# Kernel optimization log

Measured on AMD Instinct MI355X. Metric: run time of the kernel, lower is better.

Reference implementation:

```python
import jax, jax.numpy as jnp
import numpy as np

N = 50000
E = 800000
IN_FEATS = 128
OUT_FEATS = 64
ALPHA = 0.2  # LeakyReLU negative slope


def setup_inputs() -> dict:
    key = jax.random.key(0)
    k1, k2, k3, k4, k5 = jax.random.split(key, 5)
    h = jax.random.normal(k1, (N, IN_FEATS), dtype=jnp.float32)
    src = jax.random.randint(k2, (E,), 0, N)
    dst = jax.random.randint(k3, (E,), 0, N)
    edge_index = jnp.stack([src, dst], axis=0).astype(jnp.int64)
    # xavier_uniform with gain=1.414
    limW = 1.414 * np.sqrt(6.0 / (IN_FEATS + OUT_FEATS))
    W = jax.random.uniform(k4, (IN_FEATS, OUT_FEATS), dtype=jnp.float32, minval=-limW, maxval=limW)
    lima = 1.414 * np.sqrt(6.0 / (2 * OUT_FEATS + 1))
    a = jax.random.uniform(k5, (2 * OUT_FEATS, 1), dtype=jnp.float32, minval=-lima, maxval=lima)
    return {"h": h, "edge_index": edge_index, "W": W, "a": a}


def reference(h, edge_index, W, a):
    src, dst = edge_index[0], edge_index[1]
    Wh = h @ W                               # (N, out)
    # split attention vector: cat([Wh_src, Wh_dst]) @ a == Wh_src@a1 + Wh_dst@a2
    a1 = a[:OUT_FEATS, 0]                    # (out,)
    a2 = a[OUT_FEATS:, 0]                    # (out,)
    s1 = Wh @ a1                             # (N,)
    s2 = Wh @ a2                             # (N,)
    e = jax.nn.leaky_relu(s1[src] + s2[dst], negative_slope=ALPHA)  # (E,)
    exp_e = jnp.exp(e)
    denom = jax.ops.segment_sum(exp_e, dst, num_segments=N)          # (N,)
    attention = exp_e / denom[dst]                                   # (E,)
    # dropout p=0.0 / eval mode -> identity
    msgs = attention[:, None] * Wh[src]                              # (E, out)
    h_prime = jax.ops.segment_sum(msgs, dst, num_segments=N)         # (N, out)
    return jax.nn.elu(h_prime)
```

## Files before the change

### kernel.cpp

```cpp
#include <hip/hip_runtime.h>
#include <math.h>

#define GN 50000
#define GE 800000
#define INF 128
#define OUTF 64
#define LRELU_ALPHA 0.2f

#define BUCK_SH 6
#define BUCKW   64
#define NB      ((GN + BUCKW - 1) / BUCKW)
#define CHUNK   4096
#define NCH     ((GE + CHUNK - 1) / CHUNK)
#define CAP     1536

__device__ __forceinline__ unsigned short f32_to_bf16(float f) {
    unsigned int u = __float_as_uint(f);
    return (unsigned short)((u + 0x7fffu + ((u >> 16) & 1u)) >> 16);
}
__device__ __forceinline__ float bf16lo(unsigned int u) { return __uint_as_float(u << 16); }
__device__ __forceinline__ float bf16hi(unsigned int u) { return __uint_as_float(u & 0xffff0000u); }

__global__ __launch_bounds__(256) void k_front(const float* __restrict__ h,
                                               const float* __restrict__ W,
                                               const float* __restrict__ a,
                                               const int* __restrict__ src,
                                               const int* __restrict__ dst,
                                               unsigned short* __restrict__ Whb,
                                               float* __restrict__ s1,
                                               float* __restrict__ s2,
                                               int* __restrict__ ccount,
                                               int* __restrict__ epacked) {
    __shared__ __align__(16) float Wlds[INF * OUTF];
    int t = threadIdx.x;

    if (blockIdx.x < NB) {
        for (int i = t * 4; i < INF * OUTF; i += 256 * 4)
            *(float4*)&Wlds[i] = *(const float4*)&W[i];
        __syncthreads();

        int fg = t & 15;
        int ng = t >> 4;
        int jg = fg * 4;
        int n0 = blockIdx.x * 64 + ng * 4;

        int m0 = n0 + 0 < GN ? n0 + 0 : GN - 1;
        int m1 = n0 + 1 < GN ? n0 + 1 : GN - 1;
        int m2 = n0 + 2 < GN ? n0 + 2 : GN - 1;
        int m3 = n0 + 3 < GN ? n0 + 3 : GN - 1;
        const float* h0 = &h[m0 * INF];
        const float* h1 = &h[m1 * INF];
        const float* h2 = &h[m2 * INF];
        const float* h3 = &h[m3 * INF];

        float4 acc0 = {0.f,0.f,0.f,0.f}, acc1 = acc0, acc2 = acc0, acc3 = acc0;
        for (int kc = 0; kc < INF; kc += 4) {
            float4 hv0 = *(const float4*)&h0[kc];
            float4 hv1 = *(const float4*)&h1[kc];
            float4 hv2 = *(const float4*)&h2[kc];
            float4 hv3 = *(const float4*)&h3[kc];
            #pragma unroll
            for (int kk = 0; kk < 4; ++kk) {
                float4 wv = *(float4*)&Wlds[(kc + kk) * OUTF + jg];
                float a0 = ((const float*)&hv0)[kk];
                float a1v = ((const float*)&hv1)[kk];
                float a2v = ((const float*)&hv2)[kk];
                float a3 = ((const float*)&hv3)[kk];
                acc0.x += a0 * wv.x; acc0.y += a0 * wv.y; acc0.z += a0 * wv.z; acc0.w += a0 * wv.w;
                acc1.x += a1v * wv.x; acc1.y += a1v * wv.y; acc1.z += a1v * wv.z; acc1.w += a1v * wv.w;
                acc2.x += a2v * wv.x; acc2.y += a2v * wv.y; acc2.z += a2v * wv.z; acc2.w += a2v * wv.w;
                acc3.x += a3 * wv.x; acc3.y += a3 * wv.y; acc3.z += a3 * wv.z; acc3.w += a3 * wv.w;
            }
        }

        float4 accs[4] = {acc0, acc1, acc2, acc3};
        #pragma unroll
        for (int i = 0; i < 4; ++i) {
            if (n0 + i < GN) {
                ushort4 p;
                p.x = f32_to_bf16(accs[i].x); p.y = f32_to_bf16(accs[i].y);
                p.z = f32_to_bf16(accs[i].z); p.w = f32_to_bf16(accs[i].w);
                *(ushort4*)&Whb[(n0 + i) * OUTF + jg] = p;
            }
        }

        float4 va1 = *(const float4*)&a[jg];
        float4 va2 = *(const float4*)&a[OUTF + jg];
        float p1[4], p2[4];
        #pragma unroll
        for (int i = 0; i < 4; ++i) {
            p1[i] = accs[i].x * va1.x + accs[i].y * va1.y + accs[i].z * va1.z + accs[i].w * va1.w;
            p2[i] = accs[i].x * va2.x + accs[i].y * va2.y + accs[i].z * va2.z + accs[i].w * va2.w;
        }
        #pragma unroll
        for (int off = 8; off >= 1; off >>= 1) {
            #pragma unroll
            for (int i = 0; i < 4; ++i) {
                p1[i] += __shfl_down(p1[i], off, 16);
                p2[i] += __shfl_down(p2[i], off, 16);
            }
        }
        if (fg == 0) {
            #pragma unroll
            for (int i = 0; i < 4; ++i) {
                if (n0 + i < GN) { s1[n0 + i] = p1[i]; s2[n0 + i] = p2[i]; }
            }
        }
    } else {
        int* hist = (int*)Wlds;
        int* run  = hist + NB;
        for (int i = t; i < NB; i += 256) hist[i] = 0;
        __syncthreads();

        int base = (blockIdx.x - NB) * CHUNK;
        int pk[CHUNK / 256];
        int bb[CHUNK / 256];
        #pragma unroll
        for (int i = 0; i < CHUNK / 256; ++i) {
            int e = base + i * 256 + t;
            if (e < GE) {
                int d = dst[e];
                int b = d >> BUCK_SH;
                pk[i] = (src[e] << BUCK_SH) | (d & (BUCKW - 1));
                bb[i] = b;
                atomicAdd(&hist[b], 1);
            } else {
                bb[i] = -1;
            }
        }
        __syncthreads();
        for (int i = t; i < NB; i += 256) {
            int c = hist[i];
            if (c > 0) run[i] = i * CAP + atomicAdd(&ccount[i], c);
        }
        __syncthreads();
        #pragma unroll
        for (int i = 0; i < CHUNK / 256; ++i) {
            if (bb[i] >= 0) {
                int pos = atomicAdd(&run[bb[i]], 1);
                epacked[pos] = pk[i];
            }
        }
    }
}

__global__ __launch_bounds__(256) void k_fgather(const int* __restrict__ ccount,
                                                 const int* __restrict__ epacked,
                                                 const float* __restrict__ s1,
                                                 const float* __restrict__ s2,
                                                 const unsigned short* __restrict__ Whb,
                                                 float* __restrict__ out) {
    __shared__ int elds[CAP];
    __shared__ int sorted[CAP];
    __shared__ float exs[CAP];
    __shared__ int hist[BUCKW];
    __shared__ int cur[BUCKW];
    __shared__ int cstart[BUCKW + 1];
    __shared__ float s2l[BUCKW];

    int t = threadIdx.x;
    int b = blockIdx.x;
    int dstbase = b * BUCKW;
    int nd = GN - dstbase; if (nd > BUCKW) nd = BUCKW;

    int start = b * CAP;
    int cnt   = ccount[b];
    if (cnt > CAP) cnt = CAP;

    if (t < BUCKW) {
        hist[t] = 0;
        s2l[t] = (t < nd) ? s2[dstbase + t] : 0.f;
    }
    __syncthreads();

    float exr[CAP / 256];
    #pragma unroll
    for (int it = 0; it < CAP / 256; ++it) {
        int i = t + it * 256;
        if (i < cnt) {
            int pk = epacked[start + i];
            elds[i] = pk;
            atomicAdd(&hist[pk & (BUCKW - 1)], 1);
            float x = s1[pk >> BUCK_SH] + s2l[pk & (BUCKW - 1)];
            x = (x > 0.f) ? x : LRELU_ALPHA * x;
            exr[it] = __expf(x);
        }
    }
    __syncthreads();
    if (t < 64) {
        int v = hist[t];
        int incl = v;
        #pragma unroll
        for (int off = 1; off < 64; off <<= 1) {
            int u = __shfl_up(incl, off, 64);
            if (t >= off) incl += u;
        }
        cstart[t + 1] = incl;
        cur[t] = incl - v;
        if (t == 0) cstart[0] = 0;
    }
    __syncthreads();
    #pragma unroll
    for (int it = 0; it < CAP / 256; ++it) {
        int i = t + it * 256;
        if (i < cnt) {
            int pk = elds[i];
            int pos = atomicAdd(&cur[pk & (BUCKW - 1)], 1);
            sorted[pos] = pk;
            exs[pos] = exr[it];
        }
    }
    __syncthreads();

    int grp  = t >> 3;
    int lane = t & 7;
    int jg   = lane * 8;
    for (int dl = grp; dl < BUCKW; dl += 32) {
        int c0 = cstart[dl], c1 = cstart[dl + 1];
        float acc[8] = {0.f,0.f,0.f,0.f,0.f,0.f,0.f,0.f};
        float den = 0.f;
        for (int cb = c0; cb < c1; cb += 8) {
            int m = c1 - cb; if (m > 8) m = 8;
            int   sj[8]; float exj[8];
            #pragma unroll
            for (int j = 0; j < 8; ++j) {
                if (j < m) {
                    int pk = sorted[cb + j];
                    sj[j]  = pk >> BUCK_SH;
                    exj[j] = exs[cb + j];
                }
            }
            uint4 wv[8];
            #pragma unroll
            for (int j = 0; j < 8; ++j)
                if (j < m) wv[j] = *(const uint4*)&Whb[sj[j] * OUTF + jg];
            #pragma unroll
            for (int j = 0; j < 8; ++j) {
                if (j < m) {
                    float ex = exj[j];
                    den += ex;
                    acc[0] += ex * bf16lo(wv[j].x); acc[1] += ex * bf16hi(wv[j].x);
                    acc[2] += ex * bf16lo(wv[j].y); acc[3] += ex * bf16hi(wv[j].y);
                    acc[4] += ex * bf16lo(wv[j].z); acc[5] += ex * bf16hi(wv[j].z);
                    acc[6] += ex * bf16lo(wv[j].w); acc[7] += ex * bf16hi(wv[j].w);
                }
            }
        }
        if (dl < nd) {
            float inv = (c1 > c0) ? 1.f / den : 0.f;
            float o[8];
            #pragma unroll
            for (int j = 0; j < 8; ++j) {
                float v = acc[j] * inv;
                o[j] = (v > 0.f) ? v : expm1f(v);
            }
            float* op = &out[(dstbase + dl) * OUTF + jg];
            *(float4*)(op + 0) = make_float4(o[0], o[1], o[2], o[3]);
            *(float4*)(op + 4) = make_float4(o[4], o[5], o[6], o[7]);
        }
    }
}

extern "C" void kernel_launch(void* const* d_in, const int* in_sizes, int n_in,
                              void* d_out, int out_size, void* d_ws, size_t ws_size,
                              hipStream_t stream) {
    const float* h  = (const float*)d_in[0];
    const int*   ei = (const int*)d_in[1];
    const float* W  = (const float*)d_in[2];
    const float* a  = (const float*)d_in[3];
    const int* src = ei;
    const int* dst = ei + GE;

    float* ws = (float*)d_ws;
    float* s1 = ws;
    float* s2 = s1 + GN;
    unsigned short* Whb = (unsigned short*)(s2 + GN);
    int* epacked = (int*)(Whb + (size_t)GN * OUTF);
    int* ccount  = epacked + (size_t)NB * CAP;
    float* out = (float*)d_out;

    hipMemsetAsync(ccount, 0, NB * sizeof(int), stream);
    k_front<<<NB + NCH, 256, 0, stream>>>(h, W, a, src, dst, Whb, s1, s2,
                                          ccount, epacked);
    k_fgather<<<NB, 256, 0, stream>>>(ccount, epacked, s1, s2, Whb, out);
}
```

Baseline: 132.6 us.

## Replace global atomic bucket reservation with fixed per-chunk slots and histogram matrix

Each edge-chunk block now writes its packed edges into a fixed slot region (bucket x chunk x 28) and records per-chunk counts in a 2D histogram. This removes the global atomicAdd on bucket counters and the memset launch that zeroed them. The gather kernel prefix-sums the per-chunk counts to compact the edges, and it packs the edge key and exp value together as int2. Chunk blocks are now scheduled before the node-transform blocks. In exchange, the workspace is much larger and sparse. The gather must scan 5488 slot positions per bucket, and edges are silently dropped if one chunk ever puts more than 28 into a single bucket.

```diff
diff --git a/kernel.cpp b/kernel.cpp
--- a/kernel.cpp
+++ b/kernel.cpp
@@ -12,7 +12,9 @@
 #define NB      ((GN + BUCKW - 1) / BUCKW)
 #define CHUNK   4096
 #define NCH     ((GE + CHUNK - 1) / CHUNK)
-#define CAP     1536
+#define CAP2    28
+#define ROWW    (NCH * CAP2)
+#define CAPB    1536
 
 __device__ __forceinline__ unsigned short f32_to_bf16(float f) {
     unsigned int u = __float_as_uint(f);
@@ -29,12 +31,36 @@
                                                unsigned short* __restrict__ Whb,
                                                float* __restrict__ s1,
                                                float* __restrict__ s2,
-                                               int* __restrict__ ccount,
+                                               int* __restrict__ hist2d,
                                                int* __restrict__ epacked) {
     __shared__ __align__(16) float Wlds[INF * OUTF];
     int t = threadIdx.x;
 
-    if (blockIdx.x < NB) {
+    if (blockIdx.x < NCH) {
+        int* hist = (int*)Wlds;
+        for (int i = t; i < NB; i += 256) hist[i] = 0;
+        __syncthreads();
+
+        int c = blockIdx.x;
+        int base = c * CHUNK;
+        #pragma unroll
+        for (int i = 0; i < CHUNK / 256; ++i) {
+            int e = base + i * 256 + t;
+            if (e < GE) {
+                int d = dst[e];
+                int b = d >> BUCK_SH;
+                int pk = (src[e] << BUCK_SH) | (d & (BUCKW - 1));
+                int r = atomicAdd(&hist[b], 1);
+                if (r < CAP2)
+                    epacked[b * ROWW + c * CAP2 + r] = pk;
+            }
+        }
+        __syncthreads();
+        for (int i = t; i < NB; i += 256) {
+            int v = hist[i]; if (v > CAP2) v = CAP2;
+            hist2d[i * NCH + c] = v;
+        }
+    } else {
         for (int i = t * 4; i < INF * OUTF; i += 256 * 4)
             *(float4*)&Wlds[i] = *(const float4*)&W[i];
         __syncthreads();
@@ -42,7 +68,7 @@
         int fg = t & 15;
         int ng = t >> 4;
         int jg = fg * 4;
-        int n0 = blockIdx.x * 64 + ng * 4;
+        int n0 = (blockIdx.x - NCH) * 64 + ng * 4;
 
         int m0 = n0 + 0 < GN ? n0 + 0 : GN - 1;
         int m1 = n0 + 1 < GN ? n0 + 1 : GN - 1;
@@ -106,53 +132,19 @@
                 if (n0 + i < GN) { s1[n0 + i] = p1[i]; s2[n0 + i] = p2[i]; }
             }
         }
-    } else {
-        int* hist = (int*)Wlds;
-        int* run  = hist + NB;
-        for (int i = t; i < NB; i += 256) hist[i] = 0;
-        __syncthreads();
-
-        int base = (blockIdx.x - NB) * CHUNK;
-        int pk[CHUNK / 256];
-        int bb[CHUNK / 256];
-        #pragma unroll
-        for (int i = 0; i < CHUNK / 256; ++i) {
-            int e = base + i * 256 + t;
-            if (e < GE) {
-                int d = dst[e];
-                int b = d >> BUCK_SH;
-                pk[i] = (src[e] << BUCK_SH) | (d & (BUCKW - 1));
-                bb[i] = b;
-                atomicAdd(&hist[b], 1);
-            } else {
-                bb[i] = -1;
-            }
-        }
-        __syncthreads();
-        for (int i = t; i < NB; i += 256) {
-            int c = hist[i];
-            if (c > 0) run[i] = i * CAP + atomicAdd(&ccount[i], c);
-        }
-        __syncthreads();
-        #pragma unroll
-        for (int i = 0; i < CHUNK / 256; ++i) {
-            if (bb[i] >= 0) {
-                int pos = atomicAdd(&run[bb[i]], 1);
-                epacked[pos] = pk[i];
-            }
-        }
     }
 }
 
-__global__ __launch_bounds__(256) void k_fgather(const int* __restrict__ ccount,
+__global__ __launch_bounds__(256) void k_fgather(const int* __restrict__ hist2d,
                                                  const int* __restrict__ epacked,
                                                  const float* __restrict__ s1,
                                                  const float* __restrict__ s2,
                                                  const unsigned short* __restrict__ Whb,
                                                  float* __restrict__ out) {
-    __shared__ int elds[CAP];
-    __shared__ int sorted[CAP];
-    __shared__ float exs[CAP];
+    __shared__ int2 elds2[CAPB];
+    __shared__ int2 sorted2[CAPB];
+    __shared__ int cntl[NCH];
+    __shared__ int cstart2[NCH + 1];
     __shared__ int hist[BUCKW];
     __shared__ int cur[BUCKW];
     __shared__ int cstart[BUCKW + 1];
@@ -163,30 +155,57 @@
     int dstbase = b * BUCKW;
     int nd = GN - dstbase; if (nd > BUCKW) nd = BUCKW;
 
-    int start = b * CAP;
-    int cnt   = ccount[b];
-    if (cnt > CAP) cnt = CAP;
-
     if (t < BUCKW) {
         hist[t] = 0;
         s2l[t] = (t < nd) ? s2[dstbase + t] : 0.f;
     }
-    __syncthreads();
-
-    float exr[CAP / 256];
-    #pragma unroll
-    for (int it = 0; it < CAP / 256; ++it) {
-        int i = t + it * 256;
-        if (i < cnt) {
-            int pk = epacked[start + i];
-            elds[i] = pk;
-            atomicAdd(&hist[pk & (BUCKW - 1)], 1);
-            float x = s1[pk >> BUCK_SH] + s2l[pk & (BUCKW - 1)];
-            x = (x > 0.f) ? x : LRELU_ALPHA * x;
-            exr[it] = __expf(x);
-        }
-    }
-    __syncthreads();
+    for (int i = t; i < NCH; i += 256) cntl[i] = hist2d[b * NCH + i];
+    __syncthreads();
+
+    if (t < 64) {
+        int v[4]; int s = 0;
+        #pragma unroll
+        for (int k = 0; k < 4; ++k) {
+            int c = t * 4 + k;
+            v[k] = (c < NCH) ? cntl[c] : 0;
+            s += v[k];
+        }
+        int incl = s;
+        #pragma unroll
+        for (int off = 1; off < 64; off <<= 1) {
+            int u = __shfl_up(incl, off, 64);
+            if (t >= off) incl += u;
+        }
+        int excl = incl - s;
+        #pragma unroll
+        for (int k = 0; k < 4; ++k) {
+            int c = t * 4 + k;
+            if (c < NCH) cstart2[c] = excl;
+            excl += v[k];
+        }
+        if (t == 63) cstart2[NCH] = incl;
+    }
+    __syncthreads();
+    int cnt = cstart2[NCH]; if (cnt > CAPB) cnt = CAPB;
+
+    const int* row = &epacked[(size_t)b * ROWW];
+    #pragma unroll 4
+    for (int idx = t; idx < ROWW; idx += 256) {
+        int c = idx / CAP2;
+        int i = idx - c * CAP2;
+        if (i < cntl[c]) {
+            int pos = cstart2[c] + i;
+            if (pos < CAPB) {
+                int pk = row[idx];
+                atomicAdd(&hist[pk & (BUCKW - 1)], 1);
+                float x = s1[pk >> BUCK_SH] + s2l[pk & (BUCKW - 1)];
+                x = (x > 0.f) ? x : LRELU_ALPHA * x;
+                elds2[pos] = make_int2(pk, __float_as_int(__expf(x)));
+            }
+        }
+    }
+    __syncthreads();
+
     if (t < 64) {
         int v = hist[t];
         int incl = v;
@@ -200,15 +219,11 @@
         if (t == 0) cstart[0] = 0;
     }
     __syncthreads();
-    #pragma unroll
-    for (int it = 0; it < CAP / 256; ++it) {
-        int i = t + it * 256;
-        if (i < cnt) {
-            int pk = elds[i];
-            int pos = atomicAdd(&cur[pk & (BUCKW - 1)], 1);
-            sorted[pos] = pk;
-            exs[pos] = exr[it];
-        }
+
+    for (int i = t; i < cnt; i += 256) {
+        int2 pe = elds2[i];
+        int pos = atomicAdd(&cur[pe.x & (BUCKW - 1)], 1);
+        sorted2[pos] = pe;
     }
     __syncthreads();
 
@@ -225,9 +240,9 @@
             #pragma unroll
             for (int j = 0; j < 8; ++j) {
                 if (j < m) {
-                    int pk = sorted[cb + j];
-                    sj[j]  = pk >> BUCK_SH;
-                    exj[j] = exs[cb + j];
+                    int2 pe = sorted2[cb + j];
+                    sj[j]  = pe.x >> BUCK_SH;
+                    exj[j] = __uint_as_float(pe.y);
                 }
             }
             uint4 wv[8];
@@ -276,11 +291,10 @@
     float* s2 = s1 + GN;
     unsigned short* Whb = (unsigned short*)(s2 + GN);
     int* epacked = (int*)(Whb + (size_t)GN * OUTF);
-    int* ccount  = epacked + (size_t)NB * CAP;
+    int* hist2d  = epacked + (size_t)NB * ROWW;
     float* out = (float*)d_out;
 
-    hipMemsetAsync(ccount, 0, NB * sizeof(int), stream);
     k_front<<<NB + NCH, 256, 0, stream>>>(h, W, a, src, dst, Whb, s1, s2,
-                                          ccount, epacked);
-    k_fgather<<<NB, 256, 0, stream>>>(ccount, epacked, s1, s2, Whb, out);
+                                          hist2d, epacked);
+    k_fgather<<<NB, 256, 0, stream>>>(hist2d, epacked, s1, s2, Whb, out);
 }
```

Result: slower. 144.6 us (+9.0%).

## Halve destination bucket width, reorder front blocks, pack sorted edges in LDS

Applied to the files above, without the earlier changes.

Destination buckets shrink from 64 to 32 nodes (CAP 768), so the gather kernel launches twice as many blocks, each needing less LDS, which may raise occupancy and spread the work across CUs better. Each 8-thread group now handles exactly one destination. The front kernel puts the edge-bucketing blocks before the GEMM blocks so they are scheduled first. The gather keeps packed edges in registers and stores edge and exp value together as an int2 in LDS, removing one LDS array. The histogram needs more LDS (NB doubles to ~1563 buckets, still fits), and per-bucket overflow risk rises with the smaller CAP.

```diff
diff --git a/kernel.cpp b/kernel.cpp
--- a/kernel.cpp
+++ b/kernel.cpp
@@ -7,12 +7,13 @@
 #define OUTF 64
 #define LRELU_ALPHA 0.2f
 
-#define BUCK_SH 6
-#define BUCKW   64
+#define BUCK_SH 5
+#define BUCKW   32
 #define NB      ((GN + BUCKW - 1) / BUCKW)
+#define GT      ((GN + 63) / 64)
 #define CHUNK   4096
 #define NCH     ((GE + CHUNK - 1) / CHUNK)
-#define CAP     1536
+#define CAP     768
 
 __device__ __forceinline__ unsigned short f32_to_bf16(float f) {
     unsigned int u = __float_as_uint(f);
@@ -34,7 +35,42 @@
     __shared__ __align__(16) float Wlds[INF * OUTF];
     int t = threadIdx.x;
 
-    if (blockIdx.x < NB) {
+    if (blockIdx.x < NCH) {
+        int* hist = (int*)Wlds;
+        int* run  = hist + NB;
+        for (int i = t; i < NB; i += 256) hist[i] = 0;
+        __syncthreads();
+
+        int base = blockIdx.x * CHUNK;
+        int pk[CHUNK / 256];
+        int bb[CHUNK / 256];
+        #pragma unroll
+        for (int i = 0; i < CHUNK / 256; ++i) {
+            int e = base + i * 256 + t;
+            if (e < GE) {
+                int d = dst[e];
+                int b = d >> BUCK_SH;
+                pk[i] = (src[e] << BUCK_SH) | (d & (BUCKW - 1));
+                bb[i] = b;
+                atomicAdd(&hist[b], 1);
+            } else {
+                bb[i] = -1;
+            }
+        }
+        __syncthreads();
+        for (int i = t; i < NB; i += 256) {
+            int c = hist[i];
+            if (c > 0) run[i] = i * CAP + atomicAdd(&ccount[i], c);
+        }
+        __syncthreads();
+        #pragma unroll
+        for (int i = 0; i < CHUNK / 256; ++i) {
+            if (bb[i] >= 0) {
+                int pos = atomicAdd(&run[bb[i]], 1);
+                epacked[pos] = pk[i];
+            }
+        }
+    } else {
         for (int i = t * 4; i < INF * OUTF; i += 256 * 4)
             *(float4*)&Wlds[i] = *(const float4*)&W[i];
         __syncthreads();
@@ -42,7 +78,7 @@
         int fg = t & 15;
         int ng = t >> 4;
         int jg = fg * 4;
-        int n0 = blockIdx.x * 64 + ng * 4;
+        int n0 = (blockIdx.x - NCH) * 64 + ng * 4;
 
         int m0 = n0 + 0 < GN ? n0 + 0 : GN - 1;
         int m1 = n0 + 1 < GN ? n0 + 1 : GN - 1;
@@ -106,41 +142,6 @@
                 if (n0 + i < GN) { s1[n0 + i] = p1[i]; s2[n0 + i] = p2[i]; }
             }
         }
-    } else {
-        int* hist = (int*)Wlds;
-        int* run  = hist + NB;
-        for (int i = t; i < NB; i += 256) hist[i] = 0;
-        __syncthreads();
-
-        int base = (blockIdx.x - NB) * CHUNK;
-        int pk[CHUNK / 256];
-        int bb[CHUNK / 256];
-        #pragma unroll
-        for (int i = 0; i < CHUNK / 256; ++i) {
-            int e = base + i * 256 + t;
-            if (e < GE) {
-                int d = dst[e];
-                int b = d >> BUCK_SH;
-                pk[i] = (src[e] << BUCK_SH) | (d & (BUCKW - 1));
-                bb[i] = b;
-                atomicAdd(&hist[b], 1);
-            } else {
-                bb[i] = -1;
-            }
-        }
-        __syncthreads();
-        for (int i = t; i < NB; i += 256) {
-            int c = hist[i];
-            if (c > 0) run[i] = i * CAP + atomicAdd(&ccount[i], c);
-        }
-        __syncthreads();
-        #pragma unroll
-        for (int i = 0; i < CHUNK / 256; ++i) {
-            if (bb[i] >= 0) {
-                int pos = atomicAdd(&run[bb[i]], 1);
-                epacked[pos] = pk[i];
-            }
-        }
     }
 }
 
@@ -150,9 +151,7 @@
                                                  const float* __restrict__ s2,
                                                  const unsigned short* __restrict__ Whb,
                                                  float* __restrict__ out) {
-    __shared__ int elds[CAP];
-    __shared__ int sorted[CAP];
-    __shared__ float exs[CAP];
+    __shared__ int2 sorted2[CAP];
     __shared__ int hist[BUCKW];
     __shared__ int cur[BUCKW];
     __shared__ int cstart[BUCKW + 1];
@@ -163,23 +162,22 @@
     int dstbase = b * BUCKW;
     int nd = GN - dstbase; if (nd > BUCKW) nd = BUCKW;
 
-    int start = b * CAP;
-    int cnt   = ccount[b];
-    if (cnt > CAP) cnt = CAP;
-
     if (t < BUCKW) {
         hist[t] = 0;
         s2l[t] = (t < nd) ? s2[dstbase + t] : 0.f;
     }
     __syncthreads();
 
-    float exr[CAP / 256];
+    int cnt = ccount[b]; if (cnt > CAP) cnt = CAP;
+    const int* row = &epacked[b * CAP];
+
+    int pkr[CAP / 256]; float exr[CAP / 256];
     #pragma unroll
     for (int it = 0; it < CAP / 256; ++it) {
         int i = t + it * 256;
         if (i < cnt) {
-            int pk = epacked[start + i];
-            elds[i] = pk;
+            int pk = row[i];
+            pkr[it] = pk;
             atomicAdd(&hist[pk & (BUCKW - 1)], 1);
             float x = s1[pk >> BUCK_SH] + s2l[pk & (BUCKW - 1)];
             x = (x > 0.f) ? x : LRELU_ALPHA * x;
@@ -187,12 +185,13 @@
         }
     }
     __syncthreads();
-    if (t < 64) {
+
+    if (t < BUCKW) {
         int v = hist[t];
         int incl = v;
         #pragma unroll
-        for (int off = 1; off < 64; off <<= 1) {
-            int u = __shfl_up(incl, off, 64);
+        for (int off = 1; off < BUCKW; off <<= 1) {
+            int u = __shfl_up(incl, off, BUCKW);
             if (t >= off) incl += u;
         }
         cstart[t + 1] = incl;
@@ -200,14 +199,13 @@
         if (t == 0) cstart[0] = 0;
     }
     __syncthreads();
+
     #pragma unroll
     for (int it = 0; it < CAP / 256; ++it) {
         int i = t + it * 256;
         if (i < cnt) {
-            int pk = elds[i];
-            int pos = atomicAdd(&cur[pk & (BUCKW - 1)], 1);
-            sorted[pos] = pk;
-            exs[pos] = exr[it];
+            int pos = atomicAdd(&cur[pkr[it] & (BUCKW - 1)], 1);
+            sorted2[pos] = make_int2(pkr[it], __float_as_int(exr[it]));
         }
     }
     __syncthreads();
@@ -215,49 +213,48 @@
     int grp  = t >> 3;
     int lane = t & 7;
     int jg   = lane * 8;
-    for (int dl = grp; dl < BUCKW; dl += 32) {
-        int c0 = cstart[dl], c1 = cstart[dl + 1];
-        float acc[8] = {0.f,0.f,0.f,0.f,0.f,0.f,0.f,0.f};
-        float den = 0.f;
-        for (int cb = c0; cb < c1; cb += 8) {
-            int m = c1 - cb; if (m > 8) m = 8;
-            int   sj[8]; float exj[8];
-            #pragma unroll
-            for (int j = 0; j < 8; ++j) {
-                if (j < m) {
-                    int pk = sorted[cb + j];
-                    sj[j]  = pk >> BUCK_SH;
-                    exj[j] = exs[cb + j];
-                }
-            }
-            uint4 wv[8];
-            #pragma unroll
-            for (int j = 0; j < 8; ++j)
-                if (j < m) wv[j] = *(const uint4*)&Whb[sj[j] * OUTF + jg];
-            #pragma unroll
-            for (int j = 0; j < 8; ++j) {
-                if (j < m) {
-                    float ex = exj[j];
-                    den += ex;
-                    acc[0] += ex * bf16lo(wv[j].x); acc[1] += ex * bf16hi(wv[j].x);
-                    acc[2] += ex * bf16lo(wv[j].y); acc[3] += ex * bf16hi(wv[j].y);
-                    acc[4] += ex * bf16lo(wv[j].z); acc[5] += ex * bf16hi(wv[j].z);
-                    acc[6] += ex * bf16lo(wv[j].w); acc[7] += ex * bf16hi(wv[j].w);
-                }
-            }
-        }
-        if (dl < nd) {
-            float inv = (c1 > c0) ? 1.f / den : 0.f;
-            float o[8];
-            #pragma unroll
-            for (int j = 0; j < 8; ++j) {
-                float v = acc[j] * inv;
-                o[j] = (v > 0.f) ? v : expm1f(v);
-            }
-            float* op = &out[(dstbase + dl) * OUTF + jg];
-            *(float4*)(op + 0) = make_float4(o[0], o[1], o[2], o[3]);
-            *(float4*)(op + 4) = make_float4(o[4], o[5], o[6], o[7]);
-        }
+    int dl   = grp;
+    int c0 = cstart[dl], c1 = cstart[dl + 1];
+    float acc[8] = {0.f,0.f,0.f,0.f,0.f,0.f,0.f,0.f};
+    float den = 0.f;
+    for (int cb = c0; cb < c1; cb += 8) {
+        int m = c1 - cb; if (m > 8) m = 8;
+        int   sj[8]; float exj[8];
+        #pragma unroll
+        for (int j = 0; j < 8; ++j) {
+            if (j < m) {
+                int2 pe = sorted2[cb + j];
+                sj[j]  = pe.x >> BUCK_SH;
+                exj[j] = __uint_as_float(pe.y);
+            }
+        }
+        uint4 wv[8];
+        #pragma unroll
+        for (int j = 0; j < 8; ++j)
+            if (j < m) wv[j] = *(const uint4*)&Whb[sj[j] * OUTF + jg];
+        #pragma unroll
+        for (int j = 0; j < 8; ++j) {
+            if (j < m) {
+                float ex = exj[j];
+                den += ex;
+                acc[0] += ex * bf16lo(wv[j].x); acc[1] += ex * bf16hi(wv[j].x);
+                acc[2] += ex * bf16lo(wv[j].y); acc[3] += ex * bf16hi(wv[j].y);
+                acc[4] += ex * bf16lo(wv[j].z); acc[5] += ex * bf16hi(wv[j].z);
+                acc[6] += ex * bf16lo(wv[j].w); acc[7] += ex * bf16hi(wv[j].w);
+            }
+        }
+    }
+    if (dl < nd) {
+        float inv = (c1 > c0) ? 1.f / den : 0.f;
+        float o[8];
+        #pragma unroll
+        for (int j = 0; j < 8; ++j) {
+            float v = acc[j] * inv;
+            o[j] = (v > 0.f) ? v : expm1f(v);
+        }
+        float* op = &out[(dstbase + dl) * OUTF + jg];
+        *(float4*)(op + 0) = make_float4(o[0], o[1], o[2], o[3]);
+        *(float4*)(op + 4) = make_float4(o[4], o[5], o[6], o[7]);
     }
 }
 
@@ -280,7 +277,7 @@
     float* out = (float*)d_out;
 
     hipMemsetAsync(ccount, 0, NB * sizeof(int), stream);
-    k_front<<<NB + NCH, 256, 0, stream>>>(h, W, a, src, dst, Whb, s1, s2,
+    k_front<<<NCH + GT, 256, 0, stream>>>(h, W, a, src, dst, Whb, s1, s2,
                                           ccount, epacked);
     k_fgather<<<NB, 256, 0, stream>>>(ccount, epacked, s1, s2, Whb, out);
 }
```

Measured after the change: 120.8 us. 8.9% less time.
